# Optimization experiments

Measured on AMD Instinct MI355X. Metric: run time of the kernel, lower is better.

The kernel has to match this reference:

```python
import jax, jax.numpy as jnp
import numpy as np

B, T, D = 8, 2048, 1024  # batch, seq (== block_size), n_embd == head_size


def setup_inputs() -> dict:
    key = jax.random.key(0)
    k0, k1, k2, k3 = jax.random.split(key, 4)
    s = 1.0 / np.sqrt(D)
    return {
        "x": jax.random.normal(k0, (B, T, D), dtype=jnp.float32),
        "Wk": jax.random.normal(k1, (D, D), dtype=jnp.float32) * s,
        "Wq": jax.random.normal(k2, (D, D), dtype=jnp.float32) * s,
        "Wv": jax.random.normal(k3, (D, D), dtype=jnp.float32) * s,
    }


def reference(x, Wk, Wq, Wv):
    Bb, Tt, C = x.shape
    k = jnp.einsum("btc,ch->bth", x, Wk)
    q = jnp.einsum("btc,ch->bth", x, Wq)
    v = jnp.einsum("btc,ch->bth", x, Wv)
    # scaled dot-product scores with causal (tril) mask; scale = C**-0.5 (n_embd)
    wei = jnp.einsum("bqh,bkh->bqk", q, k) * (1.0 / jnp.sqrt(jnp.float32(C)))
    causal = jnp.tril(jnp.ones((Tt, Tt), dtype=bool))
    wei = jnp.where(causal[None, :, :], wei, jnp.float32(-jnp.inf))
    wei = jax.nn.softmax(wei, axis=-1)
    # dropout is identity in eval mode
    out = jnp.einsum("bqk,bkh->bqh", wei, v)
    return out
```

## Files before the change

### kernel.cpp

```cpp
#include <hip/hip_runtime.h>
#include <hip/hip_bf16.h>

#define BB 8
#define TT 2048
#define DD 1024

typedef __attribute__((ext_vector_type(8))) short short8;
typedef __attribute__((ext_vector_type(4))) float f32x4;
typedef __attribute__((ext_vector_type(4))) unsigned short u16x4;

__device__ inline void gload_lds16(const void* g, void* l) {
    __builtin_amdgcn_global_load_lds((const __attribute__((address_space(1))) void*)g,
                                     (__attribute__((address_space(3))) void*)l, 16, 0, 0);
}

template<int MODE, typename CT>
__device__ __forceinline__ void gemm_core(
    const __hip_bfloat16* __restrict__ A,
    const __hip_bfloat16* __restrict__ Bt,
    void* __restrict__ Cbase,
    int lda, int ldb, int ldc,
    int m0, int n0, int kmax,
    float scale, float* __restrict__ rs)
{
    __shared__ __align__(16) __hip_bfloat16 lsA[128 * 64];
    __shared__ __align__(16) __hip_bfloat16 lsB[128 * 64];

    const int t    = threadIdx.x;
    const int w    = t >> 6;
    const int l    = t & 63;
    const int quad = l >> 4;
    const int l16  = l & 15;
    const int wy   = w >> 1;
    const int wx   = w & 1;

    f32x4 acc[4][4];
#pragma unroll
    for (int i = 0; i < 4; i++)
#pragma unroll
        for (int j = 0; j < 4; j++) acc[i][j] = f32x4{0.f, 0.f, 0.f, 0.f};

    for (int k0 = 0; k0 < kmax; k0 += 64) {
#pragma unroll
        for (int p = 0; p < 4; p++) {
            int c   = p * 256 + t;
            int row = c >> 3;
            int gch = (c & 7) ^ (row & 7);
            const __hip_bfloat16* ga = A  + (size_t)(m0 + row) * lda + (k0 + gch * 8);
            const __hip_bfloat16* gb = Bt + (size_t)(n0 + row) * ldb + (k0 + gch * 8);
            char* la = (char*)lsA + p * 4096 + w * 1024;
            char* lb = (char*)lsB + p * 4096 + w * 1024;
            gload_lds16(ga, la);
            gload_lds16(gb, lb);
        }
        __syncthreads();

#pragma unroll
        for (int h = 0; h < 2; h++) {
            short8 aF[4], bF[4];
#pragma unroll
            for (int mf = 0; mf < 4; mf++) {
                int m = wy * 64 + mf * 16 + l16;
                aF[mf] = *(const short8*)((const char*)lsA + m * 128 +
                                          (((h * 4 + quad) ^ (m & 7)) * 16));
            }
#pragma unroll
            for (int nf = 0; nf < 4; nf++) {
                int n = wx * 64 + nf * 16 + l16;
                bF[nf] = *(const short8*)((const char*)lsB + n * 128 +
                                          (((h * 4 + quad) ^ (n & 7)) * 16));
            }
#pragma unroll
            for (int mf = 0; mf < 4; mf++)
#pragma unroll
                for (int nf = 0; nf < 4; nf++)
                    acc[mf][nf] = __builtin_amdgcn_mfma_f32_16x16x32_bf16(
                        aF[mf], bF[nf], acc[mf][nf], 0, 0, 0);
        }
        __syncthreads();
    }

    if constexpr (MODE == 0) {
        CT* C = (CT*)Cbase;
#pragma unroll
        for (int mf = 0; mf < 4; mf++) {
            int rbase = m0 + wy * 64 + mf * 16 + quad * 4;
#pragma unroll
            for (int nf = 0; nf < 4; nf++) {
                int col = n0 + wx * 64 + nf * 16 + l16;
#pragma unroll
                for (int r = 0; r < 4; r++) {
                    float v = acc[mf][nf][r] * scale;
                    if constexpr (sizeof(CT) == 2)
                        C[(size_t)(rbase + r) * ldc + col] = (CT)__float2bfloat16(v);
                    else
                        *((float*)&C[(size_t)(rbase + r) * ldc + col]) = v;
                }
            }
        }
    } else if constexpr (MODE == 1) {
        __hip_bfloat16* C = (__hip_bfloat16*)Cbase;
#pragma unroll
        for (int mf = 0; mf < 4; mf++) {
            int rbase = m0 + wy * 64 + mf * 16 + quad * 4;
#pragma unroll
            for (int r = 0; r < 4; r++) {
                int row = rbase + r;
                float part = 0.f, pv[4];
#pragma unroll
                for (int nf = 0; nf < 4; nf++) {
                    int col = n0 + wx * 64 + nf * 16 + l16;
                    float e = (col <= row) ? __expf(acc[mf][nf][r] * scale) : 0.f;
                    pv[nf] = e;
                    part += e;
                }
                part += __shfl_xor(part, 1, 64);
                part += __shfl_xor(part, 2, 64);
                part += __shfl_xor(part, 4, 64);
                part += __shfl_xor(part, 8, 64);
                if (l16 == 0) atomicAdd(&rs[row], part);
#pragma unroll
                for (int nf = 0; nf < 4; nf++) {
                    int col = n0 + wx * 64 + nf * 16 + l16;
                    C[(size_t)row * ldc + col] = __float2bfloat16(pv[nf]);
                }
            }
        }
    } else {
        float* C = (float*)Cbase;
#pragma unroll
        for (int mf = 0; mf < 4; mf++) {
            int rbase = m0 + wy * 64 + mf * 16 + quad * 4;
#pragma unroll
            for (int r = 0; r < 4; r++) {
                int row = rbase + r;
                float inv = 1.f / rs[row];
#pragma unroll
                for (int nf = 0; nf < 4; nf++) {
                    int col = n0 + wx * 64 + nf * 16 + l16;
                    C[(size_t)row * ldc + col] = acc[mf][nf][r] * inv;
                }
            }
        }
    }
}

__global__ __launch_bounds__(256, 3) void proj3(
    const __hip_bfloat16* __restrict__ xb,
    const __hip_bfloat16* __restrict__ wt,
    __hip_bfloat16* __restrict__ kq,
    __hip_bfloat16* __restrict__ vT2)
{
    const int z = blockIdx.z;
    const __hip_bfloat16 *A, *Bt;
    void* C;
    int ldc, m0, n0;
    if (z < 2) {
        A = xb; Bt = wt + z * 1048576; C = kq + (size_t)z * 16777216;
        ldc = 1024; m0 = blockIdx.x * 128; n0 = blockIdx.y * 128;
    } else {
        A = wt + 2 * 1048576; Bt = xb; C = vT2;
        ldc = 16384; m0 = blockIdx.y * 128; n0 = blockIdx.x * 128;
    }
    gemm_core<0, __hip_bfloat16>(A, Bt, C, 1024, 1024, ldc, m0, n0, 1024, 1.0f, nullptr);
}

template<int MODE, typename CT>
__global__ __launch_bounds__(256, 3) void gemm_bt(
    const __hip_bfloat16* __restrict__ Abase,
    const __hip_bfloat16* __restrict__ Btbase,
    void* __restrict__ Cbase,
    int K, int lda, int ldb, int ldc,
    long long sA, long long sB, long long sC,
    float scale, int causalSkip, int causalKStop, int swapMN, int permX,
    float* __restrict__ aux)
{
    int bx = blockIdx.x;
    if (permX) bx = (bx < 8) ? 15 - bx : bx - 8;
    const int m0 = (swapMN ? bx : blockIdx.y) * 128;
    const int n0 = (swapMN ? blockIdx.y : bx) * 128;
    if (causalSkip && n0 > m0) return;

    const int z = blockIdx.z;
    int kmax = K;
    if (causalKStop) { int km = m0 + 128; kmax = km < K ? km : K; }

    gemm_core<MODE, CT>(Abase + (size_t)z * sA, Btbase + (size_t)z * sB,
                        (char*)Cbase + (size_t)z * sC * sizeof(CT),
                        lda, ldb, ldc, m0, n0, kmax, scale,
                        aux ? aux + (size_t)z * TT : nullptr);
}

__global__ __launch_bounds__(256) void cvt_x(const float* __restrict__ in,
                                             unsigned short* __restrict__ out)
{
    size_t i = ((size_t)blockIdx.x * 256 + threadIdx.x) * 4;
    float4 f = *(const float4*)(in + i);
    union { u16x4 u; __hip_bfloat16 h[4]; } o;
    o.h[0] = __float2bfloat16(f.x);
    o.h[1] = __float2bfloat16(f.y);
    o.h[2] = __float2bfloat16(f.z);
    o.h[3] = __float2bfloat16(f.w);
    *(u16x4*)(out + i) = o.u;
}

__global__ __launch_bounds__(256) void transpose_cvt_w(
    const float* __restrict__ Wk, const float* __restrict__ Wq,
    const float* __restrict__ Wv, __hip_bfloat16* __restrict__ Wt)
{
    const float* W = blockIdx.z == 0 ? Wk : (blockIdx.z == 1 ? Wq : Wv);
    __hip_bfloat16* o = Wt + (size_t)blockIdx.z * DD * DD;
    int h0 = blockIdx.x * 32, c0 = blockIdx.y * 32;
    __shared__ float tl[32][33];
    int tx = threadIdx.x, ty = threadIdx.y;
#pragma unroll
    for (int k = 0; k < 4; k++)
        tl[ty + 8 * k][tx] = W[(size_t)(c0 + ty + 8 * k) * DD + h0 + tx];
    __syncthreads();
#pragma unroll
    for (int k = 0; k < 4; k++)
        o[(size_t)(h0 + ty + 8 * k) * DD + c0 + tx] = __float2bfloat16(tl[tx][ty + 8 * k]);
}

extern "C" void kernel_launch(void* const* d_in, const int* in_sizes, int n_in,
                              void* d_out, int out_size, void* d_ws, size_t ws_size,
                              hipStream_t stream)
{
    const float* x  = (const float*)d_in[0];
    const float* Wk = (const float*)d_in[1];
    const float* Wq = (const float*)d_in[2];
    const float* Wv = (const float*)d_in[3];
    float* out = (float*)d_out;

    char* ws = (char*)d_ws;
    __hip_bfloat16* kk   = (__hip_bfloat16*)ws;
    __hip_bfloat16* qq   = (__hip_bfloat16*)(ws + 33554432);
    __hip_bfloat16* vT2  = (__hip_bfloat16*)(ws + 67108864);
    __hip_bfloat16* wt   = (__hip_bfloat16*)(ws + 100663296);
    float*          rsum = (float*)         (ws + 100663296);
    __hip_bfloat16* xb   = (__hip_bfloat16*)(ws + 106954752);
    __hip_bfloat16* Pp   = (__hip_bfloat16*)(ws + 106954752);

    int g = (ws_size >= 106954752ull + 8ull * 8388608ull) ? 8 : 4;

    cvt_x<<<16384, 256, 0, stream>>>(x, (unsigned short*)xb);
    transpose_cvt_w<<<dim3(32, 32, 3), dim3(32, 8), 0, stream>>>(Wk, Wq, Wv, wt);

    proj3<<<dim3(128, 8, 3), 256, 0, stream>>>(xb, wt, kk, vT2);

    for (int g0 = 0; g0 < BB; g0 += g) {
        hipMemsetAsync(rsum, 0, (size_t)g * TT * 4, stream);

        gemm_bt<1, __hip_bfloat16><<<dim3(16, 16, g), 256, 0, stream>>>(
            qq + (size_t)g0 * 2097152, kk + (size_t)g0 * 2097152, (void*)Pp,
            1024, 1024, 1024, 2048,
            2097152LL, 2097152LL, 4194304LL, 0.03125f, 1, 0, 0, 1, rsum);

        gemm_bt<2, float><<<dim3(16, 8, g), 256, 0, stream>>>(
            Pp, vT2 + (size_t)g0 * 2048, (void*)(out + (size_t)g0 * 2097152),
            2048, 2048, 16384, 1024,
            4194304LL, 2048LL, 2097152LL, 1.0f, 0, 1, 1, 1, rsum);
    }
}
```

Measured before the change: 354.9 us.

## Pack causal score tiles triangularly and launch full-batch S and PV GEMMs

Scores are now stored as packed lower-triangular 128x128 tiles, and the S kernel launches only the 136 needed tiles per batch. Previously it launched a full 16x16 grid and returned early on the upper tiles. Packing lets all 8 batches fit in the workspace, so the per-group loop and its repeated memsets are removed. The PV GEMM reads the packed tiles directly. The conversion kernels are merged into one launch, and q is staged in the output buffer to save workspace. The risk is reusing the output buffer for q, which is overwritten later, and some float sqrt math for tile indexing.

```diff
diff --git a/kernel.cpp b/kernel.cpp
--- a/kernel.cpp
+++ b/kernel.cpp
@@ -14,7 +14,7 @@
                                      (__attribute__((address_space(3))) void*)l, 16, 0, 0);
 }
 
-template<int MODE, typename CT>
+template<int MODE, typename CT, bool PACKA, bool PACKC>
 __device__ __forceinline__ void gemm_core(
     const __hip_bfloat16* __restrict__ A,
     const __hip_bfloat16* __restrict__ Bt,
@@ -46,7 +46,11 @@
             int c   = p * 256 + t;
             int row = c >> 3;
             int gch = (c & 7) ^ (row & 7);
-            const __hip_bfloat16* ga = A  + (size_t)(m0 + row) * lda + (k0 + gch * 8);
+            const __hip_bfloat16* ga;
+            if constexpr (PACKA)
+                ga = A + ((size_t)(k0 >> 7) * 16384 + row * 128 + (k0 & 64) + gch * 8);
+            else
+                ga = A + (size_t)(m0 + row) * lda + (k0 + gch * 8);
             const __hip_bfloat16* gb = Bt + (size_t)(n0 + row) * ldb + (k0 + gch * 8);
             char* la = (char*)lsA + p * 4096 + w * 1024;
             char* lb = (char*)lsB + p * 4096 + w * 1024;
@@ -102,15 +106,15 @@
         __hip_bfloat16* C = (__hip_bfloat16*)Cbase;
 #pragma unroll
         for (int mf = 0; mf < 4; mf++) {
-            int rbase = m0 + wy * 64 + mf * 16 + quad * 4;
+            int rloc0 = wy * 64 + mf * 16 + quad * 4;
 #pragma unroll
             for (int r = 0; r < 4; r++) {
-                int row = rbase + r;
+                int rloc = rloc0 + r, row = m0 + rloc;
                 float part = 0.f, pv[4];
 #pragma unroll
                 for (int nf = 0; nf < 4; nf++) {
-                    int col = n0 + wx * 64 + nf * 16 + l16;
-                    float e = (col <= row) ? __expf(acc[mf][nf][r] * scale) : 0.f;
+                    int cloc = wx * 64 + nf * 16 + l16;
+                    float e = (n0 + cloc <= row) ? __expf(acc[mf][nf][r] * scale) : 0.f;
                     pv[nf] = e;
                     part += e;
                 }
@@ -121,8 +125,11 @@
                 if (l16 == 0) atomicAdd(&rs[row], part);
 #pragma unroll
                 for (int nf = 0; nf < 4; nf++) {
-                    int col = n0 + wx * 64 + nf * 16 + l16;
-                    C[(size_t)row * ldc + col] = __float2bfloat16(pv[nf]);
+                    int cloc = wx * 64 + nf * 16 + l16;
+                    if constexpr (PACKC)
+                        C[rloc * 128 + cloc] = __float2bfloat16(pv[nf]);
+                    else
+                        C[(size_t)row * ldc + (n0 + cloc)] = __float2bfloat16(pv[nf]);
                 }
             }
         }
@@ -148,7 +155,8 @@
 __global__ __launch_bounds__(256, 3) void proj3(
     const __hip_bfloat16* __restrict__ xb,
     const __hip_bfloat16* __restrict__ wt,
-    __hip_bfloat16* __restrict__ kq,
+    __hip_bfloat16* __restrict__ kk,
+    __hip_bfloat16* __restrict__ qq,
     __hip_bfloat16* __restrict__ vT2)
 {
     const int z = blockIdx.z;
@@ -156,70 +164,91 @@
     void* C;
     int ldc, m0, n0;
     if (z < 2) {
-        A = xb; Bt = wt + z * 1048576; C = kq + (size_t)z * 16777216;
+        A = xb; Bt = wt + z * 1048576; C = z ? qq : kk;
         ldc = 1024; m0 = blockIdx.x * 128; n0 = blockIdx.y * 128;
     } else {
         A = wt + 2 * 1048576; Bt = xb; C = vT2;
         ldc = 16384; m0 = blockIdx.y * 128; n0 = blockIdx.x * 128;
     }
-    gemm_core<0, __hip_bfloat16>(A, Bt, C, 1024, 1024, ldc, m0, n0, 1024, 1.0f, nullptr);
-}
-
-template<int MODE, typename CT>
-__global__ __launch_bounds__(256, 3) void gemm_bt(
-    const __hip_bfloat16* __restrict__ Abase,
-    const __hip_bfloat16* __restrict__ Btbase,
-    void* __restrict__ Cbase,
-    int K, int lda, int ldb, int ldc,
-    long long sA, long long sB, long long sC,
-    float scale, int causalSkip, int causalKStop, int swapMN, int permX,
-    float* __restrict__ aux)
+    gemm_core<0, __hip_bfloat16, false, false>(A, Bt, C, 1024, 1024, ldc,
+                                               m0, n0, 1024, 1.0f, nullptr);
+}
+
+#define TRI(i) ((i) * ((i) + 1) / 2)
+
+__global__ __launch_bounds__(256, 3) void s_gemm(
+    const __hip_bfloat16* __restrict__ qq,
+    const __hip_bfloat16* __restrict__ kk,
+    __hip_bfloat16* __restrict__ Pp,
+    float* __restrict__ rsum)
 {
     int bx = blockIdx.x;
-    if (permX) bx = (bx < 8) ? 15 - bx : bx - 8;
-    const int m0 = (swapMN ? bx : blockIdx.y) * 128;
-    const int n0 = (swapMN ? blockIdx.y : bx) * 128;
-    if (causalSkip && n0 > m0) return;
-
-    const int z = blockIdx.z;
-    int kmax = K;
-    if (causalKStop) { int km = m0 + 128; kmax = km < K ? km : K; }
-
-    gemm_core<MODE, CT>(Abase + (size_t)z * sA, Btbase + (size_t)z * sB,
-                        (char*)Cbase + (size_t)z * sC * sizeof(CT),
-                        lda, ldb, ldc, m0, n0, kmax, scale,
-                        aux ? aux + (size_t)z * TT : nullptr);
-}
-
-__global__ __launch_bounds__(256) void cvt_x(const float* __restrict__ in,
-                                             unsigned short* __restrict__ out)
-{
-    size_t i = ((size_t)blockIdx.x * 256 + threadIdx.x) * 4;
-    float4 f = *(const float4*)(in + i);
-    union { u16x4 u; __hip_bfloat16 h[4]; } o;
-    o.h[0] = __float2bfloat16(f.x);
-    o.h[1] = __float2bfloat16(f.y);
-    o.h[2] = __float2bfloat16(f.z);
-    o.h[3] = __float2bfloat16(f.w);
-    *(u16x4*)(out + i) = o.u;
-}
-
-__global__ __launch_bounds__(256) void transpose_cvt_w(
+    int mi = (int)((sqrtf(8.f * bx + 1.f) - 1.f) * 0.5f);
+    if (TRI(mi + 1) <= bx) mi++;
+    else if (TRI(mi) > bx) mi--;
+    int ni = bx - TRI(mi);
+    int z = blockIdx.y;
+
+    gemm_core<1, __hip_bfloat16, false, true>(
+        qq + (size_t)z * 2097152, kk + (size_t)z * 2097152,
+        Pp + (size_t)z * 2228224 + (size_t)(TRI(mi) + ni) * 16384,
+        1024, 1024, 0, mi * 128, ni * 128, 1024,
+        0.03125f, rsum + (size_t)z * TT);
+}
+
+__global__ __launch_bounds__(256, 3) void pv_gemm(
+    const __hip_bfloat16* __restrict__ Pp,
+    const __hip_bfloat16* __restrict__ vT2,
+    float* __restrict__ out,
+    float* __restrict__ rsum)
+{
+    int bx = blockIdx.x;
+    int mi = (bx < 8) ? 15 - bx : bx - 8;
+    int m0 = mi * 128;
+    int z = blockIdx.z;
+
+    gemm_core<2, float, true, false>(
+        Pp + (size_t)z * 2228224 + (size_t)TRI(mi) * 16384,
+        vT2 + (size_t)z * 2048,
+        out + (size_t)z * 2097152,
+        0, 16384, 1024, m0, blockIdx.y * 128, m0 + 128,
+        1.0f, rsum + (size_t)z * TT);
+}
+
+__global__ __launch_bounds__(256) void cvt_all(
+    const float* __restrict__ x,
     const float* __restrict__ Wk, const float* __restrict__ Wq,
-    const float* __restrict__ Wv, __hip_bfloat16* __restrict__ Wt)
-{
-    const float* W = blockIdx.z == 0 ? Wk : (blockIdx.z == 1 ? Wq : Wv);
-    __hip_bfloat16* o = Wt + (size_t)blockIdx.z * DD * DD;
-    int h0 = blockIdx.x * 32, c0 = blockIdx.y * 32;
-    __shared__ float tl[32][33];
-    int tx = threadIdx.x, ty = threadIdx.y;
-#pragma unroll
-    for (int k = 0; k < 4; k++)
-        tl[ty + 8 * k][tx] = W[(size_t)(c0 + ty + 8 * k) * DD + h0 + tx];
-    __syncthreads();
-#pragma unroll
-    for (int k = 0; k < 4; k++)
-        o[(size_t)(h0 + ty + 8 * k) * DD + c0 + tx] = __float2bfloat16(tl[tx][ty + 8 * k]);
+    const float* __restrict__ Wv,
+    unsigned short* __restrict__ xb, __hip_bfloat16* __restrict__ wt)
+{
+    int b = blockIdx.x;
+    if (b < 16384) {
+        size_t i = ((size_t)b * 256 + threadIdx.x) * 4;
+        float4 f = *(const float4*)(x + i);
+        union { u16x4 u; __hip_bfloat16 h[4]; } o;
+        o.h[0] = __float2bfloat16(f.x);
+        o.h[1] = __float2bfloat16(f.y);
+        o.h[2] = __float2bfloat16(f.z);
+        o.h[3] = __float2bfloat16(f.w);
+        *(u16x4*)(xb + i) = o.u;
+    } else {
+        int bb = b - 16384;
+        int zz = bb >> 10;
+        int r  = bb & 1023;
+        const float* W = zz == 0 ? Wk : (zz == 1 ? Wq : Wv);
+        __hip_bfloat16* o = wt + (size_t)zz * DD * DD;
+        int h0 = (r & 31) * 32, c0 = (r >> 5) * 32;
+        __shared__ float tl[32][33];
+        int tx = threadIdx.x & 31, ty = threadIdx.x >> 5;
+#pragma unroll
+        for (int k = 0; k < 4; k++)
+            tl[ty + 8 * k][tx] = W[(size_t)(c0 + ty + 8 * k) * DD + h0 + tx];
+        __syncthreads();
+#pragma unroll
+        for (int k = 0; k < 4; k++)
+            o[(size_t)(h0 + ty + 8 * k) * DD + c0 + tx] =
+                __float2bfloat16(tl[tx][ty + 8 * k]);
+    }
 }
 
 extern "C" void kernel_launch(void* const* d_in, const int* in_sizes, int n_in,
@@ -233,32 +262,22 @@
     float* out = (float*)d_out;
 
     char* ws = (char*)d_ws;
-    __hip_bfloat16* kk   = (__hip_bfloat16*)ws;
-    __hip_bfloat16* qq   = (__hip_bfloat16*)(ws + 33554432);
-    __hip_bfloat16* vT2  = (__hip_bfloat16*)(ws + 67108864);
-    __hip_bfloat16* wt   = (__hip_bfloat16*)(ws + 100663296);
-    float*          rsum = (float*)         (ws + 100663296);
-    __hip_bfloat16* xb   = (__hip_bfloat16*)(ws + 106954752);
-    __hip_bfloat16* Pp   = (__hip_bfloat16*)(ws + 106954752);
-
-    int g = (ws_size >= 106954752ull + 8ull * 8388608ull) ? 8 : 4;
-
-    cvt_x<<<16384, 256, 0, stream>>>(x, (unsigned short*)xb);
-    transpose_cvt_w<<<dim3(32, 32, 3), dim3(32, 8), 0, stream>>>(Wk, Wq, Wv, wt);
-
-    proj3<<<dim3(128, 8, 3), 256, 0, stream>>>(xb, wt, kk, vT2);
-
-    for (int g0 = 0; g0 < BB; g0 += g) {
-        hipMemsetAsync(rsum, 0, (size_t)g * TT * 4, stream);
-
-        gemm_bt<1, __hip_bfloat16><<<dim3(16, 16, g), 256, 0, stream>>>(
-            qq + (size_t)g0 * 2097152, kk + (size_t)g0 * 2097152, (void*)Pp,
-            1024, 1024, 1024, 2048,
-            2097152LL, 2097152LL, 4194304LL, 0.03125f, 1, 0, 0, 1, rsum);
-
-        gemm_bt<2, float><<<dim3(16, 8, g), 256, 0, stream>>>(
-            Pp, vT2 + (size_t)g0 * 2048, (void*)(out + (size_t)g0 * 2097152),
-            2048, 2048, 16384, 1024,
-            4194304LL, 2048LL, 2097152LL, 1.0f, 0, 1, 1, 1, rsum);
-    }
-}
+    __hip_bfloat16* xb   = (__hip_bfloat16*)ws;
+    __hip_bfloat16* Pp   = (__hip_bfloat16*)ws;
+    __hip_bfloat16* wt   = (__hip_bfloat16*)(ws + 35651584);
+    float*          rsum = (float*)         (ws + 35651584);
+    __hip_bfloat16* kk   = (__hip_bfloat16*)(ws + 41943040);
+    __hip_bfloat16* vT2  = (__hip_bfloat16*)(ws + 75497472);
+    __hip_bfloat16* qq   = (__hip_bfloat16*)d_out;
+
+    cvt_all<<<16384 + 3072, 256, 0, stream>>>(x, Wk, Wq, Wv,
+                                              (unsigned short*)xb, wt);
+
+    proj3<<<dim3(128, 8, 3), 256, 0, stream>>>(xb, wt, kk, qq, vT2);
+
+    hipMemsetAsync(rsum, 0, (size_t)BB * TT * 4, stream);
+
+    s_gemm<<<dim3(136, 8), 256, 0, stream>>>(qq, kk, Pp, rsum);
+
+    pv_gemm<<<dim3(16, 8, 8), 256, 0, stream>>>(Pp, vT2, out, rsum);
+}
```

New measurement: 368.2 us. +3.7%, slower.
